# Kernel optimization log

Hardware: AMD Instinct MI355X
Metric: run time of the kernel (lower is better)

Reference implementation:

```python
import jax, jax.numpy as jnp
import numpy as np

N_ATOMS = 25000
IN_FEATURES = 128
OUT_FEATURES = 128
N_SPECIES = 64


def setup_inputs() -> dict:
    key = jax.random.key(0)
    k1, k2, k3, k4 = jax.random.split(key, 4)
    features = jax.random.normal(k1, (N_ATOMS, IN_FEATURES), dtype=jnp.float32)
    species_idx = jax.random.randint(k2, (N_ATOMS,), 0, N_SPECIES, dtype=jnp.int64)
    # kaiming_uniform_ with a=sqrt(5) on fan_in gives bound = 1/sqrt(fan_in);
    # bias init uses the same bound.
    bound = 1.0 / np.sqrt(IN_FEATURES)
    weight = jax.random.uniform(
        k3, (N_SPECIES, OUT_FEATURES, IN_FEATURES), dtype=jnp.float32,
        minval=-bound, maxval=bound)
    bias = jax.random.uniform(
        k4, (N_SPECIES, OUT_FEATURES), dtype=jnp.float32,
        minval=-bound, maxval=bound)
    return {"features": features, "species_idx": species_idx,
            "weight": weight, "bias": bias}


def reference(features, species_idx, weight, bias):
    # Species-indexed weight gather + per-atom GEMV (batched matmul with q=1).
    # W[idx]: (n_atoms, out_features, in_features)
    W = jnp.take(weight, species_idx, axis=0)
    b = jnp.take(bias, species_idx, axis=0)  # (n_atoms, out_features)
    out = jnp.einsum("ni,noi->no", features, W) + b
    return out
```

## Files before the change

kernel.cpp:

```cpp
#include <hip/hip_runtime.h>

#define NATOMS 25000
#define NSP 64
#define NRANGE 8
#define RSIZE ((NATOMS + NRANGE - 1) / NRANGE)
#define NWAVE 4
#define WSUB ((RSIZE + NWAVE - 1) / NWAVE)
#define WIT ((WSUB + 63) / 64)
#define LCAP (WIT * 64)

typedef short bf16x8 __attribute__((ext_vector_type(8)));
typedef float f32x4  __attribute__((ext_vector_type(4)));
typedef unsigned short u16;
typedef __attribute__((address_space(3))) unsigned int lds_u32;
typedef __attribute__((address_space(1))) unsigned int gbl_u32;

__device__ __forceinline__ u16 f2bf(float f) {
  unsigned u = __float_as_uint(f);
  u += 0x7fffu + ((u >> 16) & 1u);
  return (u16)(u >> 16);
}

__global__ __launch_bounds__(256)
void conv_w(const float* __restrict__ w, u16* __restrict__ wbf) {
  int g = blockIdx.x * 256 + threadIdx.x;
  const float4* p = (const float4*)w + (size_t)g * 2;
  float4 v0 = p[0], v1 = p[1];
  union { u16 h[8]; bf16x8 v; } uu;
  uu.h[0] = f2bf(v0.x); uu.h[1] = f2bf(v0.y);
  uu.h[2] = f2bf(v0.z); uu.h[3] = f2bf(v0.w);
  uu.h[4] = f2bf(v1.x); uu.h[5] = f2bf(v1.y);
  uu.h[6] = f2bf(v1.z); uu.h[7] = f2bf(v1.w);
  ((bf16x8*)wbf)[g] = uu.v;
}

__global__ __launch_bounds__(256)
void zcl_main(const float* __restrict__ feat, const int* __restrict__ sp,
              const u16* __restrict__ wbf, const float* __restrict__ bias,
              float* __restrict__ out)
{
  __shared__ u16 Ws[128 * 128];
  __shared__ u16 wlist[NWAVE][LCAP];

  const int tid = threadIdx.x, bid = blockIdx.x;
  const int s = (bid & 7) + 8 * ((bid >> 3) & 7);
  const int r = bid >> 6;
  const int lo = r * RSIZE;
  const int hi = (lo + RSIZE < NATOMS) ? (lo + RSIZE) : NATOMS;

  const int wv = tid >> 6, lane = tid & 63;
  const int l16 = lane & 15, kq = lane >> 4;
  const int wlo = lo + wv * WSUB;
  const int whi = (wlo + WSUB < hi) ? (wlo + WSUB) : hi;

  int spv[WIT];
  #pragma unroll
  for (int i = 0; i < WIT; ++i) {
    int a = wlo + i * 64 + lane;
    spv[i] = (a < whi) ? sp[a] : -1;
  }

  const u16* wsrc = wbf + (size_t)s * 16384;
  #pragma unroll
  for (int rnd = 0; rnd < 8; ++rnd) {
    int m = rnd * 256 + tid, row = m >> 4, c = m & 15;
    const u16* src = wsrc + row * 128 + ((c ^ (row & 7)) << 3);
    u16* dst = &Ws[(rnd * 256 + (tid & ~63)) * 8];
    __builtin_amdgcn_global_load_lds((gbl_u32*)src, (lds_u32*)dst, 16, 0, 0);
  }

  int wcnt = 0;
  #pragma unroll
  for (int i = 0; i < WIT; ++i) {
    bool m = (spv[i] == s);
    unsigned long long mk = __ballot(m);
    if (m) wlist[wv][wcnt + __popcll(mk & ((1ull << lane) - 1ull))] =
             (u16)(wlo + i * 64 + lane);
    wcnt += (int)__popcll(mk);
  }
  const int nt = (wcnt + 15) >> 4;

  float4 pf[8];
  if (nt > 0) {
    int atomA = wlist[wv][l16 < wcnt ? l16 : 0];
    const float4* xg = (const float4*)(feat + (size_t)atomA * 128);
    #pragma unroll
    for (int ks = 0; ks < 4; ++ks) {
      pf[2 * ks]     = xg[ks * 8 + kq * 2];
      pf[2 * ks + 1] = xg[ks * 8 + kq * 2 + 1];
    }
  }

  __syncthreads();

  float bvb[8];
  #pragma unroll
  for (int nf = 0; nf < 8; ++nf) bvb[nf] = bias[s * 128 + l16 + 16 * nf];

  for (int t = 0; t < nt; ++t) {
    bf16x8 av[4];
    #pragma unroll
    for (int ks = 0; ks < 4; ++ks) {
      union { u16 h[8]; bf16x8 v; } uu;
      uu.h[0] = f2bf(pf[2 * ks].x);     uu.h[1] = f2bf(pf[2 * ks].y);
      uu.h[2] = f2bf(pf[2 * ks].z);     uu.h[3] = f2bf(pf[2 * ks].w);
      uu.h[4] = f2bf(pf[2 * ks + 1].x); uu.h[5] = f2bf(pf[2 * ks + 1].y);
      uu.h[6] = f2bf(pf[2 * ks + 1].z); uu.h[7] = f2bf(pf[2 * ks + 1].w);
      av[ks] = uu.v;
    }

    if (t + 1 < nt) {
      int li = (t + 1) * 16 + l16;
      int atomA = wlist[wv][li < wcnt ? li : 0];
      const float4* xg = (const float4*)(feat + (size_t)atomA * 128);
      #pragma unroll
      for (int ks = 0; ks < 4; ++ks) {
        pf[2 * ks]     = xg[ks * 8 + kq * 2];
        pf[2 * ks + 1] = xg[ks * 8 + kq * 2 + 1];
      }
    }

    f32x4 acc[8];
    #pragma unroll
    for (int nf = 0; nf < 8; ++nf) acc[nf] = (f32x4){0.f, 0.f, 0.f, 0.f};
    #pragma unroll
    for (int ks = 0; ks < 4; ++ks) {
      int chunk = ((ks * 4 + kq) ^ (l16 & 7)) << 3;
      #pragma unroll
      for (int nf = 0; nf < 8; ++nf) {
        bf16x8 b = *(const bf16x8*)&Ws[(l16 + 16 * nf) * 128 + chunk];
        acc[nf] = __builtin_amdgcn_mfma_f32_16x16x32_bf16(av[ks], b, acc[nf], 0, 0, 0);
      }
    }

    #pragma unroll
    for (int q = 0; q < 4; ++q) {
      int li2 = t * 16 + kq * 4 + q;
      if (li2 < wcnt) {
        int atom = wlist[wv][li2];
        float* op = out + (size_t)atom * 128 + l16;
        #pragma unroll
        for (int nf = 0; nf < 8; ++nf) op[16 * nf] = acc[nf][q] + bvb[nf];
      }
    }
  }
}

extern "C" void kernel_launch(void* const* d_in, const int* in_sizes, int n_in,
                              void* d_out, int out_size, void* d_ws, size_t ws_size,
                              hipStream_t stream) {
  const float* feat   = (const float*)d_in[0];
  const int*   sp     = (const int*)d_in[1];
  const float* weight = (const float*)d_in[2];
  const float* bias   = (const float*)d_in[3];
  float*       out    = (float*)d_out;
  u16*         wbf    = (u16*)d_ws;

  conv_w<<<512, 256, 0, stream>>>(weight, wbf);
  zcl_main<<<NSP * NRANGE, 256, 0, stream>>>(feat, sp, wbf, bias, out);
}
```

Measured before the change: 18.41 us.

## Use block-wide atomic compaction and stream weights from global instead of LDS

The atom range is split into 16 parts instead of 8, doubling the grid. The per-wave compaction lists are replaced by one block-level list built with an LDS atomic counter, and 16-atom tiles are spread round-robin across waves. The LDS staging of the species weight tile is removed, so MFMA B operands are read directly from global (L2/L1 cached) bf16 weights. This cuts LDS use and the staging cost but adds global weight traffic per tile and drops the feature prefetch pipelining.

Measured after the change: 29.03 us. +57.7%, slower.

```diff
diff --git a/kernel.cpp b/kernel.cpp
--- a/kernel.cpp
+++ b/kernel.cpp
@@ -2,18 +2,14 @@
 
 #define NATOMS 25000
 #define NSP 64
-#define NRANGE 8
+#define NRANGE 16
 #define RSIZE ((NATOMS + NRANGE - 1) / NRANGE)
-#define NWAVE 4
-#define WSUB ((RSIZE + NWAVE - 1) / NWAVE)
-#define WIT ((WSUB + 63) / 64)
-#define LCAP (WIT * 64)
+#define SCAN_IT ((RSIZE + 255) / 256)
+#define LCAP ((RSIZE + 31) & ~31)
 
 typedef short bf16x8 __attribute__((ext_vector_type(8)));
 typedef float f32x4  __attribute__((ext_vector_type(4)));
 typedef unsigned short u16;
-typedef __attribute__((address_space(3))) unsigned int lds_u32;
-typedef __attribute__((address_space(1))) unsigned int gbl_u32;
 
 __device__ __forceinline__ u16 f2bf(float f) {
   unsigned u = __float_as_uint(f);
@@ -39,65 +35,59 @@
               const u16* __restrict__ wbf, const float* __restrict__ bias,
               float* __restrict__ out)
 {
-  __shared__ u16 Ws[128 * 128];
-  __shared__ u16 wlist[NWAVE][LCAP];
+  __shared__ u16 list[LCAP];
+  __shared__ int nM;
 
   const int tid = threadIdx.x, bid = blockIdx.x;
-  const int s = (bid & 7) + 8 * ((bid >> 3) & 7);
+  const int s = bid & 63;
   const int r = bid >> 6;
   const int lo = r * RSIZE;
   const int hi = (lo + RSIZE < NATOMS) ? (lo + RSIZE) : NATOMS;
 
   const int wv = tid >> 6, lane = tid & 63;
   const int l16 = lane & 15, kq = lane >> 4;
-  const int wlo = lo + wv * WSUB;
-  const int whi = (wlo + WSUB < hi) ? (wlo + WSUB) : hi;
 
-  int spv[WIT];
+  int spv[SCAN_IT];
   #pragma unroll
-  for (int i = 0; i < WIT; ++i) {
-    int a = wlo + i * 64 + lane;
-    spv[i] = (a < whi) ? sp[a] : -1;
+  for (int i = 0; i < SCAN_IT; ++i) {
+    int a = lo + i * 256 + tid;
+    spv[i] = (a < hi) ? sp[a] : -1;
   }
 
-  const u16* wsrc = wbf + (size_t)s * 16384;
+  float bvb[8];
   #pragma unroll
-  for (int rnd = 0; rnd < 8; ++rnd) {
-    int m = rnd * 256 + tid, row = m >> 4, c = m & 15;
-    const u16* src = wsrc + row * 128 + ((c ^ (row & 7)) << 3);
-    u16* dst = &Ws[(rnd * 256 + (tid & ~63)) * 8];
-    __builtin_amdgcn_global_load_lds((gbl_u32*)src, (lds_u32*)dst, 16, 0, 0);
-  }
+  for (int nf = 0; nf < 8; ++nf) bvb[nf] = bias[s * 128 + l16 + 16 * nf];
 
-  int wcnt = 0;
+  if (tid == 0) nM = 0;
+  __syncthreads();
+
   #pragma unroll
-  for (int i = 0; i < WIT; ++i) {
+  for (int i = 0; i < SCAN_IT; ++i) {
     bool m = (spv[i] == s);
     unsigned long long mk = __ballot(m);
-    if (m) wlist[wv][wcnt + __popcll(mk & ((1ull << lane) - 1ull))] =
-             (u16)(wlo + i * 64 + lane);
-    wcnt += (int)__popcll(mk);
+    int base = 0;
+    if (lane == 0) base = atomicAdd(&nM, (int)__popcll(mk));
+    base = __shfl(base, 0);
+    if (m) list[base + __popcll(mk & ((1ull << lane) - 1ull))] =
+             (u16)(lo + i * 256 + tid);
   }
-  const int nt = (wcnt + 15) >> 4;
+  __syncthreads();
 
-  float4 pf[8];
-  if (nt > 0) {
-    int atomA = wlist[wv][l16 < wcnt ? l16 : 0];
+  const int nMatch = nM;
+  const int nt = (nMatch + 15) >> 4;
+  const u16* wsrc = wbf + (size_t)s * 16384;
+
+  for (int t = wv; t < nt; t += 4) {
+    int li = t * 16 + l16;
+    int atomA = list[li < nMatch ? li : 0];
     const float4* xg = (const float4*)(feat + (size_t)atomA * 128);
+    float4 pf[8];
     #pragma unroll
     for (int ks = 0; ks < 4; ++ks) {
       pf[2 * ks]     = xg[ks * 8 + kq * 2];
       pf[2 * ks + 1] = xg[ks * 8 + kq * 2 + 1];
     }
-  }
 
-  __syncthreads();
-
-  float bvb[8];
-  #pragma unroll
-  for (int nf = 0; nf < 8; ++nf) bvb[nf] = bias[s * 128 + l16 + 16 * nf];
-
-  for (int t = 0; t < nt; ++t) {
     bf16x8 av[4];
     #pragma unroll
     for (int ks = 0; ks < 4; ++ks) {
@@ -109,26 +99,14 @@
       av[ks] = uu.v;
     }
 
-    if (t + 1 < nt) {
-      int li = (t + 1) * 16 + l16;
-      int atomA = wlist[wv][li < wcnt ? li : 0];
-      const float4* xg = (const float4*)(feat + (size_t)atomA * 128);
-      #pragma unroll
-      for (int ks = 0; ks < 4; ++ks) {
-        pf[2 * ks]     = xg[ks * 8 + kq * 2];
-        pf[2 * ks + 1] = xg[ks * 8 + kq * 2 + 1];
-      }
-    }
-
     f32x4 acc[8];
     #pragma unroll
     for (int nf = 0; nf < 8; ++nf) acc[nf] = (f32x4){0.f, 0.f, 0.f, 0.f};
     #pragma unroll
     for (int ks = 0; ks < 4; ++ks) {
-      int chunk = ((ks * 4 + kq) ^ (l16 & 7)) << 3;
       #pragma unroll
       for (int nf = 0; nf < 8; ++nf) {
-        bf16x8 b = *(const bf16x8*)&Ws[(l16 + 16 * nf) * 128 + chunk];
+        bf16x8 b = *(const bf16x8*)&wsrc[(l16 + 16 * nf) * 128 + (ks * 4 + kq) * 8];
         acc[nf] = __builtin_amdgcn_mfma_f32_16x16x32_bf16(av[ks], b, acc[nf], 0, 0, 0);
       }
     }
@@ -136,8 +114,8 @@
     #pragma unroll
     for (int q = 0; q < 4; ++q) {
       int li2 = t * 16 + kq * 4 + q;
-      if (li2 < wcnt) {
-        int atom = wlist[wv][li2];
+      if (li2 < nMatch) {
+        int atom = list[li2];
         float* op = out + (size_t)atom * 128 + l16;
         #pragma unroll
         for (int nf = 0; nf < 8; ++nf) op[16 * nf] = acc[nf][q] + bvb[nf];
```
